# Kernel optimization log

Measured on AMD Instinct MI355X. Metric: run time of the kernel, lower is better.

The kernel has to match this reference:

```python
import jax, jax.numpy as jnp
import numpy as np

B, S, T, L, D, H = 32, 64, 256, 8, 128, 128
SIGNAL_SD = 1.0 - 0.001   # default signal_sds init
NOISE_SD = 0.01           # GP diagonal jitter (noise_sds) for Cholesky stability


def setup_inputs() -> dict:
    key = jax.random.key(0)
    ks = jax.random.split(key, 8)
    X = jax.random.normal(ks[0], (B, T, D), dtype=jnp.float32)
    times = (jnp.arange(T, dtype=jnp.float32) / T) * 10.0  # span [0, 10)
    log_taus = jax.random.normal(ks[1], (L,), dtype=jnp.float32) * 0.1 + jnp.log(0.5)
    log_R_diag = jax.random.normal(ks[2], (D,), dtype=jnp.float32) * 0.1
    W1 = jax.random.normal(ks[3], (L, H), dtype=jnp.float32) / np.sqrt(L)
    b1 = jnp.zeros((H,), dtype=jnp.float32)
    W2 = jax.random.normal(ks[4], (H, D), dtype=jnp.float32) / np.sqrt(H)
    b2 = jnp.zeros((D,), dtype=jnp.float32)
    eps = jax.random.normal(ks[5], (B, S, L, T), dtype=jnp.float32)
    return {"X": X, "times": times, "log_taus": log_taus, "log_R_diag": log_R_diag,
            "W1": W1, "b1": b1, "W2": W2, "b2": b2, "eps": eps}


def reference(X, times, log_taus, log_R_diag, W1, b1, W2, b2, eps):
    taus = jnp.exp(log_taus)            # [L]
    r = jnp.exp(log_R_diag)             # [D] diagonal of R

    # --- GP prior kernel matrices (squared-exponential SDE kernel), one per latent dim ---
    dt = times[:, None] - times[None, :]                       # [T,T]
    K = (SIGNAL_SD ** 2) * jnp.exp(-(dt ** 2)[None] / (2.0 * (taus ** 2)[:, None, None]))
    K = K + (NOISE_SD ** 2) * jnp.eye(T, dtype=K.dtype)        # [L,T,T]
    Lc = jnp.linalg.cholesky(K)                                # [L,T,T]

    # --- reparameterized prior samples: z = Lc @ eps ---
    z = jnp.einsum('lut,bslt->bslu', Lc, eps)                  # [B,S,L,T]
    Z = jnp.transpose(z, (0, 1, 3, 2))                         # [B,S,T,L]

    # --- decoder MLP: latent -> manifold mean in observation space ---
    h = jnp.tanh(jnp.einsum('bstl,lh->bsth', Z, W1) + b1)      # [B,S,T,H]
    mu = jnp.einsum('bsth,hd->bstd', h, W2) + b2               # [B,S,T,D]

    # --- diagonal-R Gaussian log_prob per timestep, closed form ---
    diff = X[:, None, :, :] - mu                               # [B,S,T,D]
    quad = jnp.sum(diff * diff / r, axis=-1)                   # [B,S,T]
    log_norm = 0.5 * (jnp.sum(log_R_diag) + D * jnp.log(2.0 * jnp.pi))
    logp = -0.5 * quad - log_norm                              # [B,S,T]

    # --- sum over time, logsumexp over MC samples ---
    ll = jnp.sum(logp, axis=2)                                 # [B,S]
    nll = -(jax.scipy.special.logsumexp(ll, axis=1) - jnp.log(jnp.float32(S)))
    return nll                                                 # [B]
```

## Files before the change

### kernel.cpp

```cpp
#include <hip/hip_runtime.h>
#include <hip/hip_bf16.h>
#include <math.h>

#define B_ 32
#define S_ 64
#define T_ 256
#define L_ 8
#define D_ 128
#define H_ 128

typedef __attribute__((ext_vector_type(8))) short short8;
typedef __attribute__((ext_vector_type(4))) short short4v;
typedef __attribute__((ext_vector_type(4))) float float4v;
typedef __attribute__((ext_vector_type(4))) int int4v;

__device__ __forceinline__ short f2bf(float x) {
  __hip_bfloat16 h = __float2bfloat16(x);
  return *reinterpret_cast<short*>(&h);
}

__device__ __forceinline__ float rdlane(float x, int sl) {
  return __int_as_float(__builtin_amdgcn_readlane(__float_as_int(x), sl));
}
__device__ __forceinline__ float dpp_shr1(float x, float tailv) {
  int r = __builtin_amdgcn_update_dpp(__float_as_int(tailv), __float_as_int(x),
                                      0x138, 0xF, 0xF, false);
  return __int_as_float(r);
}

__global__ __launch_bounds__(64) void k_chol_prep(
    const float* __restrict__ times, const float* __restrict__ log_taus,
    __hip_bfloat16* __restrict__ Lcbf_,
    const float* __restrict__ W1, const float* __restrict__ W2,
    __hip_bfloat16* __restrict__ W1T, __hip_bfloat16* __restrict__ W2T,
    const float* __restrict__ eps, __hip_bfloat16* __restrict__ Eg)
{
  __shared__ short panel[256][68];
  const int bi = blockIdx.x;
  const int j = threadIdx.x;

  if (bi >= 72) {
    short* EgS = (short*)Eg;
    const int e = bi - 72;
    const int sub = j >> 3, part = j & 7;
#pragma unroll 1
    for (int p = 0; p < 4; ++p) {
      const int ri = e * 32 + p * 8 + sub;
      const int l = ri & 7, bs = ri >> 3;
      const float* src = eps + (size_t)ri * 256;
      short* dst = EgS + ((size_t)(l << 11) + bs) * 256;
#pragma unroll
      for (int g = 0; g < 8; ++g) {
        const int c = (part + g * 8) * 4;
        float4v f = *(const float4v*)(src + c);
        short4v o;
#pragma unroll
        for (int jj = 0; jj < 4; ++jj) o[jj] = f2bf(f[jj]);
        *(short4v*)&dst[c] = o;
      }
    }
    return;
  }

  if (bi >= 8) {
    const int base = (bi - 8) * 64 + j;
    for (int idx = base; idx < H_ * D_; idx += 4096) {
      const int cc = idx >> 7, h = idx & 127;
      const int n = cc & 15, nt = cc >> 4;
      const int d = n * 8 + nt;
      W2T[(size_t)cc * H_ + h] = __float2bfloat16(W2[(size_t)h * D_ + d]);
    }
    for (int idx = base; idx < L_ * H_; idx += 4096) {
      const int li = idx >> 7, h = idx & 127;
      const int msrc = 32 * (h >> 5) + 2 * (h & 15) + ((h >> 4) & 1);
      W1T[(size_t)h * L_ + li] = __float2bfloat16(W1[(size_t)li * H_ + msrc]);
    }
    return;
  }

  const int l = bi;
  short* Lbf = (short*)Lcbf_ + (size_t)l * T_ * T_;

  const float tau = expf(log_taus[l]);
  const float inv2tau2 = 0.5f / (tau * tau);
  const float sig2 = 0.999f * 0.999f;
  const float t0 = times[0];

  const float c0 = sig2 + 1e-4f;
  const float isc0 = 1.0f / sqrtf(c0);

  float u[4], v[4];
#pragma unroll
  for (int c = 0; c < 4; ++c) {
    const int d = c * 64 + j;
    const float dt = times[d] - t0;
    float cv = sig2 * __expf(-dt * dt * inv2tau2);
    if (d == 0) cv = c0;
    u[c] = cv * isc0;
    v[c] = (d == 0) ? 0.0f : u[c];
  }

#pragma unroll
  for (int p = 0; p < 4; ++p) {
    for (int base = 0; base < 64; base += 8) {
      float au[8], av[8];
#pragma unroll
      for (int t = 0; t < 8; ++t) {
        au[t] = rdlane(u[p], base + t);
        av[t] = rdlane(v[p], base + t);
      }
      float s[8], sr[8];
#pragma unroll
      for (int m = 0; m < 8; ++m) {
        const float a0 = au[0], b0 = av[0];
        const float dd = fmaxf(__builtin_fmaf(a0, a0, -b0 * b0), 1e-20f);
        const float rr = __builtin_amdgcn_rsqf(dd);
        s[m] = a0 * rr;
        sr[m] = b0 * rr;
        if (m < 7) {
          float nu[7], nv[7];
#pragma unroll
          for (int t = 0; t < 7; ++t) {
            if (t < 7 - m) {
              nu[t] = s[m] * au[t] - sr[m] * av[t];
              nv[t] = s[m] * av[t + 1] - sr[m] * au[t + 1];
            }
          }
#pragma unroll
          for (int t = 0; t < 7; ++t) {
            if (t < 7 - m) { au[t] = nu[t]; av[t] = nv[t]; }
          }
        }
      }

#pragma unroll
      for (int m = 0; m < 8; ++m) {
        const int kk = base + m;
        float A[4];
#pragma unroll
        for (int c = 0; c < 4; ++c) {
          if (c >= p) {
            const float uc = u[c], vc = v[c];
            A[c] = s[m] * uc - sr[m] * vc;
            v[c] = s[m] * vc - sr[m] * uc;
            const float val = (c > p || j >= kk) ? A[c] : 0.0f;
            panel[(c - p) * 64 + j][kk] = f2bf(val);
          }
        }
#pragma unroll
        for (int c = 3; c >= 0; --c) {
          if (c >= p) {
            const float tail = (c > p) ? rdlane(A[c - 1], 63) : 0.0f;
            u[c] = dpp_shr1(A[c], tail);
          }
        }
      }
    }
    __syncthreads();
    const int rpt = 256 - 64 * p;
    const int rsub = j >> 4, cp = (j & 15) * 4;
    for (int i0 = 0; i0 < rpt; i0 += 4) {
      const int pr = i0 + rsub;
      short4v vv = *(const short4v*)&panel[pr][cp];
      *(short4v*)&Lbf[((size_t)(p * 64 + pr) << 8) + p * 64 + cp] = vv;
    }
    __syncthreads();
  }
}

__global__ __launch_bounds__(256) void k_zgemm(
    const float* __restrict__ eps, const __hip_bfloat16* __restrict__ Eg,
    const __hip_bfloat16* __restrict__ Lcbf_,
    __hip_bfloat16* __restrict__ Zg, const int useEg)
{
  __shared__ __align__(16) short E[32][264];
  const int bi = blockIdx.x;
  const int l = bi & 7, bs0 = (bi >> 3) * 32;
  const int tid = threadIdx.x, w = tid >> 6, lane = tid & 63;
  const int n = lane & 15, q = lane >> 4;
  const short* Lb = (const short*)Lcbf_ + (size_t)l * T_ * T_;

  if (!useEg) {
    const int row = tid >> 3, part = tid & 7;
    const float* src = eps + ((size_t)(bs0 + row) * L_ + l) * T_;
#pragma unroll
    for (int g = 0; g < 8; ++g) {
      const int c = (part + g * 8) * 4;
      float4v f = *(const float4v*)(src + c);
      short4v o;
#pragma unroll
      for (int jj = 0; jj < 4; ++jj) o[jj] = f2bf(f[jj]);
      *(short4v*)&E[row][c] = o;
    }
    __syncthreads();
  }

  float4v acc[4][2];
#pragma unroll
  for (int mi = 0; mi < 4; ++mi)
#pragma unroll
    for (int nt = 0; nt < 2; ++nt) acc[mi][nt] = (float4v){0.f, 0.f, 0.f, 0.f};

  const int kmax = ((15 - w + 2) >> 1) << 5;
  if (useEg) {
    const short* Eb = (const short*)Eg + ((size_t)(l << 11) + bs0) * 256;
    for (int k0 = 0; k0 < kmax; k0 += 32) {
      short8 bfrg[2];
#pragma unroll
      for (int nt = 0; nt < 2; ++nt)
        bfrg[nt] = *(const short8*)&Eb[(size_t)(nt * 16 + n) * 256 + k0 + q * 8];
#pragma unroll
      for (int mi = 0; mi < 4; ++mi) {
        const int tile = (mi == 0) ? w : (mi == 1) ? (15 - w) : (mi == 2) ? (7 - w) : (8 + w);
        const int kc = ((tile + 2) >> 1) << 5;
        if (k0 < kc) {
          const int u = tile * 16 + n;
          const short8 afr = *(const short8*)&Lb[((size_t)u << 8) + k0 + q * 8];
#pragma unroll
          for (int nt = 0; nt < 2; ++nt)
            acc[mi][nt] = __builtin_amdgcn_mfma_f32_16x16x32_bf16(afr, bfrg[nt], acc[mi][nt], 0, 0, 0);
        }
      }
    }
  } else {
    for (int k0 = 0; k0 < kmax; k0 += 32) {
      short8 bfrg[2];
#pragma unroll
      for (int nt = 0; nt < 2; ++nt)
        bfrg[nt] = *(const short8*)&E[nt * 16 + n][k0 + q * 8];
#pragma unroll
      for (int mi = 0; mi < 4; ++mi) {
        const int tile = (mi == 0) ? w : (mi == 1) ? (15 - w) : (mi == 2) ? (7 - w) : (8 + w);
        const int kc = ((tile + 2) >> 1) << 5;
        if (k0 < kc) {
          const int u = tile * 16 + n;
          const short8 afr = *(const short8*)&Lb[((size_t)u << 8) + k0 + q * 8];
#pragma unroll
          for (int nt = 0; nt < 2; ++nt)
            acc[mi][nt] = __builtin_amdgcn_mfma_f32_16x16x32_bf16(afr, bfrg[nt], acc[mi][nt], 0, 0, 0);
        }
      }
    }
  }
  __syncthreads();

#pragma unroll
  for (int mi = 0; mi < 4; ++mi) {
    const int tile = (mi == 0) ? w : (mi == 1) ? (15 - w) : (mi == 2) ? (7 - w) : (8 + w);
#pragma unroll
    for (int nt = 0; nt < 2; ++nt) {
      short4v o;
#pragma unroll
      for (int r = 0; r < 4; ++r) o[r] = f2bf(acc[mi][nt][r]);
      *(short4v*)&E[nt * 16 + n][tile * 16 + q * 4] = o;
    }
  }
  __syncthreads();

  {
    const int row = tid >> 3, part = tid & 7;
    short* dst = (short*)Zg + ((size_t)l * (B_ * S_) + bs0 + row) * T_;
#pragma unroll
    for (int g = 0; g < 4; ++g) {
      const int c = (g * 8 + part) * 8;
      *(short8*)&dst[c] = *(const short8*)&E[row][c];
    }
  }
}

__global__ __launch_bounds__(256, 4) void k_decode(
    const float* __restrict__ X, const __hip_bfloat16* __restrict__ Zg,
    const __hip_bfloat16* __restrict__ W1T, const float* __restrict__ b1,
    const __hip_bfloat16* __restrict__ W2T, const float* __restrict__ b2,
    const float* __restrict__ log_R, float* __restrict__ ll)
{
  __shared__ __align__(16) short Zt[256][8];
  __shared__ __align__(16) __hip_bfloat16 hS[32][136];
  __shared__ float redbuf[4];

  const int bid = blockIdx.x;
  const int pair = (bid & 7) * 128 + (bid >> 3);
  const int b = pair >> 5;
  const int tid = threadIdx.x;
  const int w = tid >> 6, lane = tid & 63;
  const int n = lane & 15, q = lane >> 4;
  const unsigned short* Zs = (const unsigned short*)Zg;
  const short* W1s = (const short*)W1T;
  const short* W2s = (const short*)W2T;

  float sLR = log_R[lane] + log_R[lane + 64];
#pragma unroll
  for (int off = 32; off >= 1; off >>= 1) sLR += __shfl_xor(sLR, off);

  const float L22 = 2.8853900817779268f;
  const int d0 = n * 8 + 2 * w;
  const int hc = 32 * w + 2 * n;
  float invr2[2], b22[2], pb[2];
#pragma unroll
  for (int jj = 0; jj < 2; ++jj) {
    invr2[jj] = expf(-log_R[d0 + jj]);
    b22[jj] = b2[d0 + jj];
    pb[jj] = b1[hc + jj] * L22;
  }

  const short8 zero8 = {0, 0, 0, 0, 0, 0, 0, 0};
  short8 w1f[2];
  short8 bfr[2][4];
#pragma unroll
  for (int jj = 0; jj < 2; ++jj) {
    const int c = (2 * w + jj) * 16 + n;
    short8 v = zero8;
    if (q == 0) v = *(const short8*)&W1s[(size_t)c * L_];
    w1f[jj] = v;
#pragma unroll
    for (int ks = 0; ks < 4; ++ks)
      bfr[jj][ks] = *(const short8*)&W2s[(size_t)c * H_ + ks * 32 + q * 8];
  }

  const float log_norm = 0.5f * (sLR + (float)D_ * 1.8378770664093453f);

#pragma unroll 1
  for (int bsi = 0; bsi < 2; ++bsi) {
    const int bs = pair * 2 + bsi;

    {
      const size_t base = (size_t)bs * T_ + tid;
      const size_t lstr = (size_t)(B_ * S_) * T_;
      unsigned int p0 = (unsigned int)Zs[base]            | ((unsigned int)Zs[base + lstr]     << 16);
      unsigned int p1 = (unsigned int)Zs[base + 2 * lstr] | ((unsigned int)Zs[base + 3 * lstr] << 16);
      unsigned int p2 = (unsigned int)Zs[base + 4 * lstr] | ((unsigned int)Zs[base + 5 * lstr] << 16);
      unsigned int p3 = (unsigned int)Zs[base + 6 * lstr] | ((unsigned int)Zs[base + 7 * lstr] << 16);
      int4v zi = {(int)p0, (int)p1, (int)p2, (int)p3};
      *(int4v*)&Zt[tid][0] = zi;
    }

    float qsum = 0.0f;
    __syncthreads();

#pragma unroll 1
    for (int ph = 0; ph < 8; ++ph) {
      short* hp = (short*)hS + (q * 4) * 136 + hc;
#pragma unroll 1
      for (int mi = 0; mi < 2; ++mi) {
        short8 zf = zero8;
        if (q == 0) zf = *(const short8*)&Zt[ph * 32 + mi * 16 + n][0];
        float4v c0 = __builtin_amdgcn_mfma_f32_16x16x32_bf16(zf, w1f[0], (float4v){0.f,0.f,0.f,0.f}, 0, 0, 0);
        float4v c1 = __builtin_amdgcn_mfma_f32_16x16x32_bf16(zf, w1f[1], (float4v){0.f,0.f,0.f,0.f}, 0, 0, 0);
#pragma unroll
        for (int r = 0; r < 4; ++r) {
          const float a0 = __builtin_fmaf(c0[r], L22, pb[0]);
          const float a1 = __builtin_fmaf(c1[r], L22, pb[1]);
          const float p0 = __builtin_amdgcn_exp2f(a0) + 1.f;
          const float p1 = __builtin_amdgcn_exp2f(a1) + 1.f;
          const float rj = __builtin_amdgcn_rcpf(p0 * p1);
          const float h0 = __builtin_fmaf(-2.f * p1, rj, 1.f);
          const float h1 = __builtin_fmaf(-2.f * p0, rj, 1.f);
          float2 hv2; hv2.x = h0; hv2.y = h1;
          *reinterpret_cast<__hip_bfloat162*>(hp + r * 136) = __float22bfloat162_rn(hv2);
        }
        hp += 16 * 136;
      }
      __syncthreads();
#pragma unroll 1
      for (int mi = 0; mi < 2; ++mi) {
        short8 af[4];
#pragma unroll
        for (int ks = 0; ks < 4; ++ks)
          af[ks] = *(const short8*)&hS[mi * 16 + n][ks * 32 + q * 8];
        float4v acc0 = (float4v){0.f, 0.f, 0.f, 0.f};
        float4v acc1 = (float4v){0.f, 0.f, 0.f, 0.f};
#pragma unroll
        for (int ks = 0; ks < 4; ++ks) {
          acc0 = __builtin_amdgcn_mfma_f32_16x16x32_bf16(af[ks], bfr[0][ks], acc0, 0, 0, 0);
          acc1 = __builtin_amdgcn_mfma_f32_16x16x32_bf16(af[ks], bfr[1][ks], acc1, 0, 0, 0);
        }
        const int tbase = ph * 32 + mi * 16 + q * 4;
#pragma unroll
        for (int r = 0; r < 4; ++r) {
          const int t = tbase + r;
          const float2 xv = *(const float2*)(X + (((size_t)b << 8) + t) * D_ + d0);
          float diff0 = xv.x - (acc0[r] + b22[0]);
          float diff1 = xv.y - (acc1[r] + b22[1]);
          qsum += diff0 * diff0 * invr2[0] + diff1 * diff1 * invr2[1];
        }
      }
      __syncthreads();
    }

#pragma unroll
    for (int off = 32; off >= 1; off >>= 1) qsum += __shfl_xor(qsum, off);
    if (lane == 0) redbuf[w] = qsum;
    __syncthreads();
    if (tid == 0) {
      const float Q = redbuf[0] + redbuf[1] + redbuf[2] + redbuf[3];
      ll[bs] = -0.5f * Q - (float)T_ * log_norm;
    }
  }
}

__global__ __launch_bounds__(64) void k_lse(
    const float* __restrict__ ll, float* __restrict__ out)
{
  const int b = blockIdx.x;
  const int s = threadIdx.x;
  float v = ll[b * 64 + s];
  float m = v;
#pragma unroll
  for (int off = 32; off >= 1; off >>= 1) m = fmaxf(m, __shfl_xor(m, off));
  float e = __expf(v - m);
#pragma unroll
  for (int off = 32; off >= 1; off >>= 1) e += __shfl_xor(e, off);
  if (s == 0) out[b] = -(m + __logf(e) - 4.1588830833596715f);
}

extern "C" void kernel_launch(void* const* d_in, const int* in_sizes, int n_in,
                              void* d_out, int out_size, void* d_ws, size_t ws_size,
                              hipStream_t stream) {
  const float* X        = (const float*)d_in[0];
  const float* times    = (const float*)d_in[1];
  const float* log_taus = (const float*)d_in[2];
  const float* log_R    = (const float*)d_in[3];
  const float* W1       = (const float*)d_in[4];
  const float* b1       = (const float*)d_in[5];
  const float* W2       = (const float*)d_in[6];
  const float* b2       = (const float*)d_in[7];
  const float* eps      = (const float*)d_in[8];
  float* out = (float*)d_out;

  char* ws = (char*)d_ws;
  __hip_bfloat16* Lcbf = (__hip_bfloat16*)(ws);
  __hip_bfloat16* Zg   = (__hip_bfloat16*)(ws + 1048576);
  float* ll            = (float*)(ws + 9437184);
  __hip_bfloat16* W2T  = (__hip_bfloat16*)(ws + 9445376);
  __hip_bfloat16* W1T  = (__hip_bfloat16*)(ws + 9478144);
  __hip_bfloat16* Eg   = (__hip_bfloat16*)(ws + 9480192);

  const int useEg = (ws_size >= (size_t)9480192 + 8388608) ? 1 : 0;

  hipLaunchKernelGGL(k_chol_prep, dim3(useEg ? 584 : 72), dim3(64), 0, stream,
                     times, log_taus, Lcbf, W1, W2, W1T, W2T, eps, Eg);
  hipLaunchKernelGGL(k_zgemm,     dim3(512),  dim3(256), 0, stream, eps, Eg, Lcbf, Zg, useEg);
  hipLaunchKernelGGL(k_decode,    dim3(1024), dim3(256), 0, stream, X, Zg, W1T, b1, W2T, b2, log_R, ll);
  hipLaunchKernelGGL(k_lse,       dim3(32),   dim3(64),  0, stream, ll, out);
}
```

Measured before the change: 158.8 us.

## Fuse Cholesky and Z GEMM into one kernel with per-panel flag sync

Merges the Cholesky/prep kernel and the Z = Lc·eps GEMM into a single launch. GEMM blocks convert eps to bf16 in shared memory, then spin on per-latent, per-panel release/acquire flags so they can start multiplying as soon as each 64-column panel of Lc is written. The goal is to overlap the serial Cholesky with the GEMM and drop the separate eps staging buffer and one kernel launch. In exchange it adds a memset launch and spin-waiting that relies on the Cholesky blocks being scheduled first. The Cholesky path also now runs in 256-thread blocks with four waves duplicating the same 64-lane work, and the larger combined shared-memory footprint may lower occupancy.

```diff
diff --git a/kernel.cpp b/kernel.cpp
--- a/kernel.cpp
+++ b/kernel.cpp
@@ -28,27 +28,30 @@
   return __int_as_float(r);
 }
 
-__global__ __launch_bounds__(64) void k_chol_prep(
+__global__ __launch_bounds__(256) void k_fused(
     const float* __restrict__ times, const float* __restrict__ log_taus,
     __hip_bfloat16* __restrict__ Lcbf_,
     const float* __restrict__ W1, const float* __restrict__ W2,
     __hip_bfloat16* __restrict__ W1T, __hip_bfloat16* __restrict__ W2T,
-    const float* __restrict__ eps, __hip_bfloat16* __restrict__ Eg)
+    const float* __restrict__ eps, __hip_bfloat16* __restrict__ Zg,
+    int* __restrict__ flags)
 {
   __shared__ short panel[256][68];
+  __shared__ __align__(16) short E[32][264];
   const int bi = blockIdx.x;
-  const int j = threadIdx.x;
+  const int tid = threadIdx.x;
 
   if (bi >= 72) {
-    short* EgS = (short*)Eg;
-    const int e = bi - 72;
-    const int sub = j >> 3, part = j & 7;
-#pragma unroll 1
-    for (int p = 0; p < 4; ++p) {
-      const int ri = e * 32 + p * 8 + sub;
-      const int l = ri & 7, bs = ri >> 3;
-      const float* src = eps + (size_t)ri * 256;
-      short* dst = EgS + ((size_t)(l << 11) + bs) * 256;
+    const int bi2 = bi - 72;
+    const int l = bi2 & 7, bs0 = (bi2 >> 3) * 32;
+    const int w = tid >> 6, lane = tid & 63;
+    const int n = lane & 15, q = lane >> 4;
+    const short* Lb = (const short*)Lcbf_ + (size_t)l * T_ * T_;
+    const int* fl = flags + l * 4;
+
+    {
+      const int row = tid >> 3, part = tid & 7;
+      const float* src = eps + ((size_t)(bs0 + row) * L_ + l) * T_;
 #pragma unroll
       for (int g = 0; g < 8; ++g) {
         const int c = (part + g * 8) * 4;
@@ -56,21 +59,78 @@
         short4v o;
 #pragma unroll
         for (int jj = 0; jj < 4; ++jj) o[jj] = f2bf(f[jj]);
-        *(short4v*)&dst[c] = o;
+        *(short4v*)&E[row][c] = o;
+      }
+    }
+    __syncthreads();
+
+    float4v acc[4][2];
+#pragma unroll
+    for (int mi = 0; mi < 4; ++mi)
+#pragma unroll
+      for (int nt = 0; nt < 2; ++nt) acc[mi][nt] = (float4v){0.f, 0.f, 0.f, 0.f};
+
+    const int kmax = ((15 - w + 2) >> 1) << 5;
+    for (int k0 = 0; k0 < kmax; k0 += 32) {
+      if ((k0 & 63) == 0) {
+        const int pi = k0 >> 6;
+        while (__hip_atomic_load(&fl[pi], __ATOMIC_ACQUIRE,
+                                 __HIP_MEMORY_SCOPE_AGENT) == 0)
+          __builtin_amdgcn_s_sleep(8);
+      }
+      short8 bfrg[2];
+#pragma unroll
+      for (int nt = 0; nt < 2; ++nt)
+        bfrg[nt] = *(const short8*)&E[nt * 16 + n][k0 + q * 8];
+#pragma unroll
+      for (int mi = 0; mi < 4; ++mi) {
+        const int tile = (mi == 0) ? w : (mi == 1) ? (15 - w) : (mi == 2) ? (7 - w) : (8 + w);
+        const int kc = ((tile + 2) >> 1) << 5;
+        if (k0 < kc) {
+          const int u = tile * 16 + n;
+          const short8 afr = *(const short8*)&Lb[((size_t)u << 8) + k0 + q * 8];
+#pragma unroll
+          for (int nt = 0; nt < 2; ++nt)
+            acc[mi][nt] = __builtin_amdgcn_mfma_f32_16x16x32_bf16(afr, bfrg[nt], acc[mi][nt], 0, 0, 0);
+        }
+      }
+    }
+    __syncthreads();
+
+#pragma unroll
+    for (int mi = 0; mi < 4; ++mi) {
+      const int tile = (mi == 0) ? w : (mi == 1) ? (15 - w) : (mi == 2) ? (7 - w) : (8 + w);
+#pragma unroll
+      for (int nt = 0; nt < 2; ++nt) {
+        short4v o;
+#pragma unroll
+        for (int r = 0; r < 4; ++r) o[r] = f2bf(acc[mi][nt][r]);
+        *(short4v*)&E[nt * 16 + n][tile * 16 + q * 4] = o;
+      }
+    }
+    __syncthreads();
+
+    {
+      const int row = tid >> 3, part = tid & 7;
+      short* dst = (short*)Zg + ((size_t)l * (B_ * S_) + bs0 + row) * T_;
+#pragma unroll
+      for (int g = 0; g < 4; ++g) {
+        const int c = (g * 8 + part) * 8;
+        *(short8*)&dst[c] = *(const short8*)&E[row][c];
       }
     }
     return;
   }
 
   if (bi >= 8) {
-    const int base = (bi - 8) * 64 + j;
-    for (int idx = base; idx < H_ * D_; idx += 4096) {
+    const int base = (bi - 8) * 256 + tid;
+    for (int idx = base; idx < H_ * D_; idx += 16384) {
       const int cc = idx >> 7, h = idx & 127;
       const int n = cc & 15, nt = cc >> 4;
       const int d = n * 8 + nt;
       W2T[(size_t)cc * H_ + h] = __float2bfloat16(W2[(size_t)h * D_ + d]);
     }
-    for (int idx = base; idx < L_ * H_; idx += 4096) {
+    for (int idx = base; idx < L_ * H_; idx += 16384) {
       const int li = idx >> 7, h = idx & 127;
       const int msrc = 32 * (h >> 5) + 2 * (h & 15) + ((h >> 4) & 1);
       W1T[(size_t)h * L_ + li] = __float2bfloat16(W1[(size_t)li * H_ + msrc]);
@@ -79,6 +139,7 @@
   }
 
   const int l = bi;
+  const int j = tid & 63;
   short* Lbf = (short*)Lcbf_ + (size_t)l * T_ * T_;
 
   const float tau = expf(log_taus[l]);
@@ -164,107 +225,11 @@
       short4v vv = *(const short4v*)&panel[pr][cp];
       *(short4v*)&Lbf[((size_t)(p * 64 + pr) << 8) + p * 64 + cp] = vv;
     }
-    __syncthreads();
-  }
-}
-
-__global__ __launch_bounds__(256) void k_zgemm(
-    const float* __restrict__ eps, const __hip_bfloat16* __restrict__ Eg,
-    const __hip_bfloat16* __restrict__ Lcbf_,
-    __hip_bfloat16* __restrict__ Zg, const int useEg)
-{
-  __shared__ __align__(16) short E[32][264];
-  const int bi = blockIdx.x;
-  const int l = bi & 7, bs0 = (bi >> 3) * 32;
-  const int tid = threadIdx.x, w = tid >> 6, lane = tid & 63;
-  const int n = lane & 15, q = lane >> 4;
-  const short* Lb = (const short*)Lcbf_ + (size_t)l * T_ * T_;
-
-  if (!useEg) {
-    const int row = tid >> 3, part = tid & 7;
-    const float* src = eps + ((size_t)(bs0 + row) * L_ + l) * T_;
-#pragma unroll
-    for (int g = 0; g < 8; ++g) {
-      const int c = (part + g * 8) * 4;
-      float4v f = *(const float4v*)(src + c);
-      short4v o;
-#pragma unroll
-      for (int jj = 0; jj < 4; ++jj) o[jj] = f2bf(f[jj]);
-      *(short4v*)&E[row][c] = o;
-    }
-    __syncthreads();
-  }
-
-  float4v acc[4][2];
-#pragma unroll
-  for (int mi = 0; mi < 4; ++mi)
-#pragma unroll
-    for (int nt = 0; nt < 2; ++nt) acc[mi][nt] = (float4v){0.f, 0.f, 0.f, 0.f};
-
-  const int kmax = ((15 - w + 2) >> 1) << 5;
-  if (useEg) {
-    const short* Eb = (const short*)Eg + ((size_t)(l << 11) + bs0) * 256;
-    for (int k0 = 0; k0 < kmax; k0 += 32) {
-      short8 bfrg[2];
-#pragma unroll
-      for (int nt = 0; nt < 2; ++nt)
-        bfrg[nt] = *(const short8*)&Eb[(size_t)(nt * 16 + n) * 256 + k0 + q * 8];
-#pragma unroll
-      for (int mi = 0; mi < 4; ++mi) {
-        const int tile = (mi == 0) ? w : (mi == 1) ? (15 - w) : (mi == 2) ? (7 - w) : (8 + w);
-        const int kc = ((tile + 2) >> 1) << 5;
-        if (k0 < kc) {
-          const int u = tile * 16 + n;
-          const short8 afr = *(const short8*)&Lb[((size_t)u << 8) + k0 + q * 8];
-#pragma unroll
-          for (int nt = 0; nt < 2; ++nt)
-            acc[mi][nt] = __builtin_amdgcn_mfma_f32_16x16x32_bf16(afr, bfrg[nt], acc[mi][nt], 0, 0, 0);
-        }
-      }
-    }
-  } else {
-    for (int k0 = 0; k0 < kmax; k0 += 32) {
-      short8 bfrg[2];
-#pragma unroll
-      for (int nt = 0; nt < 2; ++nt)
-        bfrg[nt] = *(const short8*)&E[nt * 16 + n][k0 + q * 8];
-#pragma unroll
-      for (int mi = 0; mi < 4; ++mi) {
-        const int tile = (mi == 0) ? w : (mi == 1) ? (15 - w) : (mi == 2) ? (7 - w) : (8 + w);
-        const int kc = ((tile + 2) >> 1) << 5;
-        if (k0 < kc) {
-          const int u = tile * 16 + n;
-          const short8 afr = *(const short8*)&Lb[((size_t)u << 8) + k0 + q * 8];
-#pragma unroll
-          for (int nt = 0; nt < 2; ++nt)
-            acc[mi][nt] = __builtin_amdgcn_mfma_f32_16x16x32_bf16(afr, bfrg[nt], acc[mi][nt], 0, 0, 0);
-        }
-      }
-    }
-  }
-  __syncthreads();
-
-#pragma unroll
-  for (int mi = 0; mi < 4; ++mi) {
-    const int tile = (mi == 0) ? w : (mi == 1) ? (15 - w) : (mi == 2) ? (7 - w) : (8 + w);
-#pragma unroll
-    for (int nt = 0; nt < 2; ++nt) {
-      short4v o;
-#pragma unroll
-      for (int r = 0; r < 4; ++r) o[r] = f2bf(acc[mi][nt][r]);
-      *(short4v*)&E[nt * 16 + n][tile * 16 + q * 4] = o;
-    }
-  }
-  __syncthreads();
-
-  {
-    const int row = tid >> 3, part = tid & 7;
-    short* dst = (short*)Zg + ((size_t)l * (B_ * S_) + bs0 + row) * T_;
-#pragma unroll
-    for (int g = 0; g < 4; ++g) {
-      const int c = (g * 8 + part) * 8;
-      *(short8*)&dst[c] = *(const short8*)&E[row][c];
-    }
+    __threadfence();
+    if (tid == 0)
+      __hip_atomic_store(&flags[l * 4 + p], 1, __ATOMIC_RELEASE,
+                         __HIP_MEMORY_SCOPE_AGENT);
+    __syncthreads();
   }
 }
 
@@ -433,13 +398,12 @@
   float* ll            = (float*)(ws + 9437184);
   __hip_bfloat16* W2T  = (__hip_bfloat16*)(ws + 9445376);
   __hip_bfloat16* W1T  = (__hip_bfloat16*)(ws + 9478144);
-  __hip_bfloat16* Eg   = (__hip_bfloat16*)(ws + 9480192);
-
-  const int useEg = (ws_size >= (size_t)9480192 + 8388608) ? 1 : 0;
-
-  hipLaunchKernelGGL(k_chol_prep, dim3(useEg ? 584 : 72), dim3(64), 0, stream,
-                     times, log_taus, Lcbf, W1, W2, W1T, W2T, eps, Eg);
-  hipLaunchKernelGGL(k_zgemm,     dim3(512),  dim3(256), 0, stream, eps, Eg, Lcbf, Zg, useEg);
-  hipLaunchKernelGGL(k_decode,    dim3(1024), dim3(256), 0, stream, X, Zg, W1T, b1, W2T, b2, log_R, ll);
-  hipLaunchKernelGGL(k_lse,       dim3(32),   dim3(64),  0, stream, ll, out);
-}
+  int* flags           = (int*)(ws + 9480192);
+
+  hipMemsetAsync(flags, 0, 32 * sizeof(int), stream);
+  hipLaunchKernelGGL(k_fused,  dim3(584),  dim3(256), 0, stream,
+                     times, log_taus, Lcbf, W1, W2, W1T, W2T, eps, Zg, flags);
+  hipLaunchKernelGGL(k_decode, dim3(1024), dim3(256), 0, stream,
+                     X, Zg, W1T, b1, W2T, b2, log_R, ll);
+  hipLaunchKernelGGL(k_lse,    dim3(32),   dim3(64),  0, stream, ll, out);
+}
```

New measurement: 262.5 us. 65.3% more time.
